# Performance work log

Measured on AMD Instinct MI355X. Metric: run time of the kernel, lower is better.

## Reference

```python
import jax, jax.numpy as jnp
import numpy as np

B, CIN, COUT, H, W, K, S, P = 16, 256, 128, 64, 64, 4, 2, 1
PAD = K - 1 - P  # transposed-conv equivalent padding for the lhs-dilated conv


def setup_inputs() -> dict:
    key = jax.random.key(0)
    ks = jax.random.split(key, 13)
    return {
        "x": jax.random.normal(ks[0], (B, CIN, H, W), jnp.float32),
        "feature": jax.random.uniform(ks[1], (B, 4), jnp.float32),
        "weight": jax.random.normal(ks[2], (CIN, COUT, K, K), jnp.float32) * 0.05,
        "t_bayer": jax.random.normal(ks[3], (1, CIN, COUT, K, K), jnp.float32) * 0.05,
        "t_quad": jax.random.normal(ks[4], (1, CIN, COUT, K, K), jnp.float32) * 0.05,
        "t_nano": jax.random.normal(ks[5], (1, CIN, COUT, K, K), jnp.float32) * 0.05,
        "t_qxq": jax.random.normal(ks[6], (1, CIN, COUT, K, K), jnp.float32) * 0.05,
        "m_bayer": jax.random.uniform(ks[7], (1, CIN, COUT, 1, 1), jnp.float32),
        "m_quad": jax.random.uniform(ks[8], (1, CIN, COUT, 1, 1), jnp.float32),
        "m_nano": jax.random.uniform(ks[9], (1, CIN, COUT, 1, 1), jnp.float32),
        "m_qxq": jax.random.uniform(ks[10], (1, CIN, COUT, 1, 1), jnp.float32),
        "bias": jax.random.normal(ks[11], (COUT,), jnp.float32) * 0.05,
        "prelu_a": jnp.full((1,), 0.25, jnp.float32),
    }


def _synth_weights(feature, weight, t_bayer, t_quad, t_nano, t_qxq,
                   m_bayer, m_quad, m_nano, m_qxq):
    # feature: (B,4) softmax attention -> (B,4,1,1,1)
    sa = feature[:, :, None, None, None]
    dyn = (t_bayer * m_bayer * sa[:, 0:1]
           + t_quad * m_quad * sa[:, 1:2]
           + t_nano * m_nano * sa[:, 2:3]
           + t_qxq * m_qxq * sa[:, 3:4])  # (B, CIN, COUT, K, K)
    return weight[None] + dyn  # broadcast base weight over batch


def _deconv_per_sample(xi, wi):
    # xi: (CIN,H,W); wi: (CIN,COUT,K,K) torch conv_transpose layout.
    # conv_transpose == lhs-dilated conv with spatially-flipped, transposed kernel
    kern = jnp.flip(jnp.swapaxes(wi, 0, 1), axis=(-2, -1))  # (COUT,CIN,K,K)
    out = jax.lax.conv_general_dilated(
        xi[None], kern, window_strides=(1, 1),
        padding=[(PAD, PAD), (PAD, PAD)], lhs_dilation=(S, S),
        dimension_numbers=("NCHW", "OIHW", "NCHW"))
    return out[0]  # (COUT, H*S, W*S)


def reference(x, feature, weight, t_bayer, t_quad, t_nano, t_qxq,
              m_bayer, m_quad, m_nano, m_qxq, bias, prelu_a):
    w = _synth_weights(feature, weight, t_bayer, t_quad, t_nano, t_qxq,
                       m_bayer, m_quad, m_nano, m_qxq)
    out = jax.vmap(_deconv_per_sample)(x, w)  # (B, COUT, 128, 128)
    out = out + bias[None, :, None, None]
    # PReLU with single shared slope (torch default init 0.25)
    return jnp.where(out >= 0, out, prelu_a[0] * out)
```

## Files before the change

kernel.cpp:

```cpp
#include <hip/hip_runtime.h>
#include <hip/hip_bf16.h>
#include <cstddef>
#include <cstdint>

#define B_    16
#define CIN_  256
#define COUT_ 128
#define H_    64
#define W_    64
#define OH_   128
#define OW_   128

typedef __attribute__((ext_vector_type(8))) short bf16x8;
typedef __attribute__((ext_vector_type(4))) float f32x4;

__device__ inline short f2bf(float f) {
    __hip_bfloat16 h = __float2bfloat16(f);
    return *reinterpret_cast<short*>(&h);
}

__device__ inline void async_ld16(const void* g, void* l) {
    typedef const __attribute__((address_space(1))) unsigned int* gp_t;
    typedef __attribute__((address_space(3))) unsigned int* lp_t;
    __builtin_amdgcn_global_load_lds((gp_t)g, (lp_t)l, 16, 0, 0);
}

__global__ __launch_bounds__(256) void synth_aws(
    const float* __restrict__ weight,
    const float* __restrict__ tb, const float* __restrict__ tq,
    const float* __restrict__ tn, const float* __restrict__ tx,
    const float* __restrict__ mb, const float* __restrict__ mq,
    const float* __restrict__ mn, const float* __restrict__ mx,
    const float* __restrict__ feat,
    short* __restrict__ aws)
{
    const int chunk = blockIdx.x;
    const int cog   = blockIdx.y;
    const int b     = blockIdx.z;
    const int tid   = threadIdx.x;
    const int ci0   = chunk * 8;

    __shared__ __align__(16) short lbuf[4][32][40];

    const float f0 = feat[b*4+0], f1 = feat[b*4+1];
    const float f2 = feat[b*4+2], f3 = feat[b*4+3];

    #pragma unroll
    for (int it = 0; it < 4; ++it) {
        int e4   = tid + it*256;
        int ci_l = e4 >> 7;
        int rem  = e4 & 127;
        int co_l = rem >> 2;
        int kh   = rem & 3;
        int co   = cog*32 + co_l;
        int base = (ci0 + ci_l) * COUT_ + co;
        float4 w4 = *(const float4*)(weight + (size_t)base*16 + kh*4);
        float4 b4 = *(const float4*)(tb + (size_t)base*16 + kh*4);
        float4 q4 = *(const float4*)(tq + (size_t)base*16 + kh*4);
        float4 n4 = *(const float4*)(tn + (size_t)base*16 + kh*4);
        float4 x4 = *(const float4*)(tx + (size_t)base*16 + kh*4);
        const float* wp = (const float*)&w4;
        const float* bp = (const float*)&b4;
        const float* qp = (const float*)&q4;
        const float* np = (const float*)&n4;
        const float* xp = (const float*)&x4;
        float sb = mb[base]*f0, sq = mq[base]*f1;
        float sn = mn[base]*f2, sx = mx[base]*f3;
        int r  = (kh+1)&1;
        int dh = (kh<2) ? 1 : 0;
        #pragma unroll
        for (int kw = 0; kw < 4; ++kw) {
            int s  = (kw+1)&1;
            int dw = (kw<2) ? 1 : 0;
            float v = wp[kw] + sb*bp[kw] + sq*qp[kw] + sn*np[kw] + sx*xp[kw];
            lbuf[r*2+s][co_l][(dh*2+dw)*8 + ci_l] = f2bf(v);
        }
    }
    __syncthreads();
    for (int j = tid; j < 640; j += 256) {
        int cls = j / 160; int jj = j - cls*160;
        size_t dst = (((size_t)(b*4 + cls)*32 + chunk)*128 + cog*32) * 40;
        *(int4*)(aws + dst + (size_t)jj*8) = *(const int4*)(&lbuf[cls][0][0] + jj*8);
    }
}

__global__ __launch_bounds__(256) void transform_x(
    const float* __restrict__ x, short* __restrict__ xt)
{
    const int ihp = blockIdx.x;
    const int b   = blockIdx.y;
    const int tid = threadIdx.x;
    const int4 z4 = {0, 0, 0, 0};

    if (ihp == 0 || ihp == 65) {
        for (int j = tid; j < 2112; j += 256) {
            int c = j / 66, iwp = j - c*66;
            *(int4*)(xt + ((((size_t)b*32 + c)*66 + ihp)*66 + iwp)*8) = z4;
        }
        return;
    }
    if (tid < 64) {
        int c = tid >> 1, iwp = (tid & 1) * 65;
        *(int4*)(xt + ((((size_t)b*32 + c)*66 + ihp)*66 + iwp)*8) = z4;
    }
    const int ih = ihp - 1;
    __shared__ float xls[128][64];
    for (int half = 0; half < 2; ++half) {
        __syncthreads();
        #pragma unroll 4
        for (int it = 0; it < 32; ++it) {
            int ci_l = it*4 + (tid >> 6);
            xls[ci_l][tid & 63] =
                x[(((size_t)b*256 + half*128 + ci_l)*64 + ih)*64 + (tid & 63)];
        }
        __syncthreads();
        #pragma unroll
        for (int it2 = 0; it2 < 4; ++it2) {
            int chunk_l = it2*4 + (tid >> 6);
            int chunk   = half*16 + chunk_l;
            int iw      = tid & 63;
            short s8[8];
            #pragma unroll
            for (int j = 0; j < 8; ++j) s8[j] = f2bf(xls[chunk_l*8 + j][iw]);
            *(int4*)(xt + ((((size_t)b*32 + chunk)*66 + ihp)*66 + (iw+1))*8)
                = *(const int4*)s8;
        }
    }
}

__global__ __launch_bounds__(256) void deconv_mfma2(
    const short* __restrict__ aws, const short* __restrict__ xt,
    const float* __restrict__ bias, const float* __restrict__ prelu_a,
    float* __restrict__ out)
{
    const int tid  = threadIdx.x;
    const int lane = tid & 63;
    const int wv   = tid >> 6;
    const int wm   = wv & 1, wn = wv >> 1;
    const int nt   = blockIdx.x;
    const int cls  = blockIdx.y;
    const int b    = blockIdx.z;
    const int a0 = (nt >> 2) * 8, c0 = (nt & 3) * 16;
    const int r = cls >> 1, s = cls & 1;

    __shared__ __align__(16) short als[2][5120];
    __shared__ __align__(16) short xsb[2][1536];

    const short* gb[4]; int gstep[4], loff[4], isB[4], act[4];
    {
        const size_t awb = (((size_t)b*4 + cls)*32) * 5120;
        #pragma unroll
        for (int i = 0; i < 4; ++i) {
            int t = wv + i*4;
            act[i] = (t < 13);
            if (t < 10) {
                gb[i]    = aws + awb + t*512 + lane*8;
                gstep[i] = 5120;  loff[i] = t*512;  isB[i] = 0;
            } else {
                int j = t - 10;
                int p = j*64 + lane; if (p > 152) p = 152;
                int row = p / 17, col = p - row*17;
                gb[i] = xt + (((size_t)b*32*66 + (a0 + r + row))*66
                              + (c0 + s + col)) * 8;
                gstep[i] = 66*66*8;  loff[i] = j*512;  isB[i] = 1;
            }
        }
    }

    f32x4 acc[4][4];
    #pragma unroll
    for (int mi = 0; mi < 4; ++mi)
        #pragma unroll
        for (int ni = 0; ni < 4; ++ni)
            acc[mi][ni] = (f32x4){0.f, 0.f, 0.f, 0.f};

    const int nlo = lane & 15;
    const int q   = lane >> 4;
    const int dh  = q >> 1, dw = q & 1;

    #pragma unroll
    for (int i = 0; i < 4; ++i)
        if (act[i])
            async_ld16(gb[i], isB[i] ? &xsb[0][loff[i]] : &als[0][loff[i]]);

    for (int c = 0; c < 32; ++c) {
        __syncthreads();
        const int sel = c & 1;
        if (c < 31) {
            const int ps = sel ^ 1;
            #pragma unroll
            for (int i = 0; i < 4; ++i)
                if (act[i])
                    async_ld16(gb[i] + (size_t)(c+1)*gstep[i],
                               isB[i] ? &xsb[ps][loff[i]] : &als[ps][loff[i]]);
        }
        bf16x8 af[4], bfr[4];
        #pragma unroll
        for (int mi = 0; mi < 4; ++mi)
            af[mi] = *(const bf16x8*)(&als[sel][(wm*64 + mi*16 + nlo)*40 + q*8]);
        #pragma unroll
        for (int ni = 0; ni < 4; ++ni) {
            int a_local = wn*4 + ni;
            bfr[ni] = *(const bf16x8*)(&xsb[sel][((a_local + dh)*17 + (nlo + dw))*8]);
        }
        #pragma unroll
        for (int mi = 0; mi < 4; ++mi)
            #pragma unroll
            for (int ni = 0; ni < 4; ++ni)
                acc[mi][ni] = __builtin_amdgcn_mfma_f32_16x16x32_bf16(
                    af[mi], bfr[ni], acc[mi][ni], 0, 0, 0);
    }

    const float pa = prelu_a[0];
    #pragma unroll
    for (int mi = 0; mi < 4; ++mi) {
        #pragma unroll
        for (int reg = 0; reg < 4; ++reg) {
            int co = wm*64 + mi*16 + q*4 + reg;
            float bv = bias[co];
            #pragma unroll
            for (int ni = 0; ni < 4; ++ni) {
                int a_local = wn*4 + ni;
                int oh = 2*(a0 + a_local) + r;
                int ow = 2*(c0 + nlo) + s;
                float v = acc[mi][ni][reg] + bv;
                v = (v >= 0.f) ? v : pa*v;
                out[(((size_t)b*COUT_ + co)*OH_ + oh)*OW_ + ow] = v;
            }
        }
    }
}

__global__ __launch_bounds__(256, 2) void deconv_mfma_gather(
    const float* __restrict__ x,
    const short* __restrict__ aws,
    const float* __restrict__ bias,
    const float* __restrict__ prelu_a,
    float* __restrict__ out)
{
    const int tid  = threadIdx.x;
    const int lane = tid & 63;
    const int wv   = tid >> 6;
    const int wm   = wv & 1, wn = wv >> 1;
    const int nt   = blockIdx.x;
    const int cls  = blockIdx.y;
    const int b    = blockIdx.z;
    const int a0 = (nt >> 2) * 8, c0 = (nt & 3) * 16;
    const int r = cls >> 1, s = cls & 1;

    __shared__ __align__(16) short xs[1280];
    __shared__ __align__(16) short als[5120];

    int goff[5], gstep[5], gok[5];
    #pragma unroll
    for (int i = 0; i < 5; ++i) {
        int e    = tid + i*256;
        int ci_l = e & 7;
        int rc   = e >> 3;
        int row  = rc / 17;
        int col  = rc - row*17;
        int ih   = a0 - 1 + r + row;
        int iw   = c0 - 1 + s + col;
        int ok   = (rc < 153) && ((unsigned)ih < (unsigned)H_)
                              && ((unsigned)iw < (unsigned)W_);
        goff[i]  = ok ? (((b*CIN_ + ci_l)*H_ + ih)*W_ + iw) : 0;
        gstep[i] = ok ? (8*H_*W_) : 0;
        gok[i]   = ok;
    }
    const size_t aws_base = (((size_t)b*4 + cls)*32) * 5120;

    f32x4 acc[4][4];
    #pragma unroll
    for (int mi = 0; mi < 4; ++mi)
        #pragma unroll
        for (int ni = 0; ni < 4; ++ni)
            acc[mi][ni] = (f32x4){0.f, 0.f, 0.f, 0.f};

    const int nlo = lane & 15;
    const int q   = lane >> 4;
    const int dh  = q >> 1, dw = q & 1;

    for (int chunk = 0; chunk < 32; ++chunk) {
        __syncthreads();
        #pragma unroll
        for (int i = 0; i < 5; ++i) {
            float v = x[goff[i] + chunk*gstep[i]];
            v = gok[i] ? v : 0.0f;
            xs[tid + i*256] = f2bf(v);
        }
        {
            const short* src = aws + aws_base + (size_t)chunk*5120;
            #pragma unroll
            for (int i = 0; i < 3; ++i) {
                int idx = wv + i*4;
                if (idx < 10)
                    async_ld16(src + idx*512 + lane*8, als + idx*512);
            }
        }
        __syncthreads();
        bf16x8 af[4], bfr[4];
        #pragma unroll
        for (int mi = 0; mi < 4; ++mi)
            af[mi] = *(const bf16x8*)(als + (wm*64 + mi*16 + nlo)*40 + q*8);
        #pragma unroll
        for (int ni = 0; ni < 4; ++ni) {
            int a_local = wn*4 + ni;
            bfr[ni] = *(const bf16x8*)(xs + ((a_local + dh)*17 + (nlo + dw))*8);
        }
        #pragma unroll
        for (int mi = 0; mi < 4; ++mi)
            #pragma unroll
            for (int ni = 0; ni < 4; ++ni)
                acc[mi][ni] = __builtin_amdgcn_mfma_f32_16x16x32_bf16(
                    af[mi], bfr[ni], acc[mi][ni], 0, 0, 0);
    }

    const float pa = prelu_a[0];
    #pragma unroll
    for (int mi = 0; mi < 4; ++mi) {
        #pragma unroll
        for (int reg = 0; reg < 4; ++reg) {
            int co = wm*64 + mi*16 + q*4 + reg;
            float bv = bias[co];
            #pragma unroll
            for (int ni = 0; ni < 4; ++ni) {
                int a_local = wn*4 + ni;
                int oh = 2*(a0 + a_local) + r;
                int ow = 2*(c0 + nlo) + s;
                float v = acc[mi][ni][reg] + bv;
                v = (v >= 0.f) ? v : pa*v;
                out[(((size_t)b*COUT_ + co)*OH_ + oh)*OW_ + ow] = v;
            }
        }
    }
}

__global__ __launch_bounds__(256) void deconv_fallback(
    const float* __restrict__ x,
    const float* __restrict__ weight,
    const float* __restrict__ tb, const float* __restrict__ tq,
    const float* __restrict__ tn, const float* __restrict__ tx,
    const float* __restrict__ mb, const float* __restrict__ mq,
    const float* __restrict__ mn, const float* __restrict__ mx,
    const float* __restrict__ feat,
    const float* __restrict__ bias, const float* __restrict__ prelu_a,
    float* __restrict__ out)
{
    const int tid    = threadIdx.x;
    const int tile   = blockIdx.x;
    const int coT    = blockIdx.y;
    const int b      = blockIdx.z;
    const int tile_h = tile >> 3, tile_w = tile & 7;
    const int a0 = tile_h * 8;
    const int c0 = tile_w * 8;
    const int co0 = coT * 64;

    const int tco = tid & 15;
    const int tpx = tid >> 4;
    const int rr  = tpx >> 2, rc = tpx & 3;

    __shared__ float xsf[4][100];
    __shared__ float wsh[4][16][64];

    float acc[4][4][4];
    #pragma unroll
    for (int i = 0; i < 4; ++i)
        #pragma unroll
        for (int j = 0; j < 4; ++j)
            #pragma unroll
            for (int c = 0; c < 4; ++c) acc[i][j][c] = 0.f;

    float f0 = feat[b*4 + 0], f1 = feat[b*4 + 1];
    float f2 = feat[b*4 + 2], f3 = feat[b*4 + 3];

    for (int chunk = 0; chunk < CIN_ / 4; ++chunk) {
        const int ci0 = chunk * 4;
        __syncthreads();
        for (int e = tid; e < 400; e += 256) {
            int ci_l = e / 100; int rem = e - ci_l * 100;
            int rI = rem / 10;  int cI = rem - rI * 10;
            int ih = a0 - 1 + rI, iw = c0 - 1 + cI;
            float v = 0.f;
            if ((unsigned)ih < (unsigned)H_ && (unsigned)iw < (unsigned)W_)
                v = x[(((size_t)b * CIN_ + ci0 + ci_l) * H_ + ih) * W_ + iw];
            xsf[ci_l][rem] = v;
        }
        #pragma unroll
        for (int k = 0; k < 4; ++k) {
            int g = tid + k * 256;
            int ci_l = g >> 8; int rrem = g & 255;
            int co_l = rrem >> 2; int tg = (rrem & 3) * 4;
            int cico = (ci0 + ci_l) * COUT_ + co0 + co_l;
            int e = cico * 16 + tg;
            float4 w  = *(const float4*)(weight + e);
            float4 vb = *(const float4*)(tb + e);
            float4 vq = *(const float4*)(tq + e);
            float4 vn = *(const float4*)(tn + e);
            float4 vx = *(const float4*)(tx + e);
            float sb = mb[cico] * f0, sq = mq[cico] * f1;
            float sn = mn[cico] * f2, sx = mx[cico] * f3;
            float4 wvv;
            wvv.x = w.x + sb*vb.x + sq*vq.x + sn*vn.x + sx*vx.x;
            wvv.y = w.y + sb*vb.y + sq*vq.y + sn*vn.y + sx*vx.y;
            wvv.z = w.z + sb*vb.z + sq*vq.z + sn*vn.z + sx*vx.z;
            wvv.w = w.w + sb*vb.w + sq*vq.w + sn*vn.w + sx*vx.w;
            wsh[ci_l][tg + 0][co_l] = wvv.x;
            wsh[ci_l][tg + 1][co_l] = wvv.y;
            wsh[ci_l][tg + 2][co_l] = wvv.z;
            wsh[ci_l][tg + 3][co_l] = wvv.w;
        }
        __syncthreads();
        #pragma unroll
        for (int ci_l = 0; ci_l < 4; ++ci_l) {
            float xpv[4][4];
            #pragma unroll
            for (int i = 0; i < 4; ++i)
                #pragma unroll
                for (int j = 0; j < 4; ++j)
                    xpv[i][j] = xsf[ci_l][(rr*2 + i) * 10 + rc*2 + j];
            #pragma unroll
            for (int kh = 0; kh < 4; ++kh) {
                const int rpar = (kh & 1) ? 0 : 1;
                const int offh = (kh == 0) ? 2 : (kh == 3) ? 0 : 1;
                #pragma unroll
                for (int kw = 0; kw < 4; ++kw) {
                    const int spar = (kw & 1) ? 0 : 1;
                    const int offw = (kw == 0) ? 2 : (kw == 3) ? 0 : 1;
                    float4 wvv = *(const float4*)&wsh[ci_l][kh*4 + kw][tco*4];
                    float wr[4] = {wvv.x, wvv.y, wvv.z, wvv.w};
                    #pragma unroll
                    for (int da = 0; da < 2; ++da)
                        #pragma unroll
                        for (int dc = 0; dc < 2; ++dc) {
                            const float xvv = xpv[da + offh][dc + offw];
                            #pragma unroll
                            for (int cc = 0; cc < 4; ++cc)
                                acc[2*da + rpar][2*dc + spar][cc] =
                                    fmaf(wr[cc], xvv, acc[2*da + rpar][2*dc + spar][cc]);
                        }
                }
            }
        }
    }
    const float pa  = prelu_a[0];
    const int oh0 = tile_h * 16 + rr * 4;
    const int ow0 = tile_w * 16 + rc * 4;
    #pragma unroll
    for (int cc = 0; cc < 4; ++cc) {
        const int co = co0 + tco * 4 + cc;
        const float bv = bias[co];
        #pragma unroll
        for (int dr = 0; dr < 4; ++dr)
            #pragma unroll
            for (int dw2 = 0; dw2 < 4; ++dw2) {
                float v = acc[dr][dw2][cc] + bv;
                v = (v >= 0.f) ? v : pa * v;
                out[(((size_t)b * COUT_ + co) * OH_ + (oh0 + dr)) * OW_ + (ow0 + dw2)] = v;
            }
    }
}

extern "C" void kernel_launch(void* const* d_in, const int* in_sizes, int n_in,
                              void* d_out, int out_size, void* d_ws, size_t ws_size,
                              hipStream_t stream) {
    (void)in_sizes; (void)n_in; (void)out_size;
    const float* x      = (const float*)d_in[0];
    const float* feat   = (const float*)d_in[1];
    const float* weight = (const float*)d_in[2];
    const float* tb     = (const float*)d_in[3];
    const float* tq     = (const float*)d_in[4];
    const float* tn     = (const float*)d_in[5];
    const float* tx     = (const float*)d_in[6];
    const float* mb     = (const float*)d_in[7];
    const float* mq     = (const float*)d_in[8];
    const float* mn     = (const float*)d_in[9];
    const float* mx     = (const float*)d_in[10];
    const float* bias   = (const float*)d_in[11];
    const float* prelu  = (const float*)d_in[12];
    float* out = (float*)d_out;

    const size_t aws_sz = (size_t)B_ * 4 * 32 * 128 * 40 * sizeof(short);
    const size_t xt_sz  = (size_t)B_ * 32 * 66 * 66 * 8 * sizeof(short);

    if (ws_size >= aws_sz + xt_sz) {
        short* aws = (short*)d_ws;
        short* xt  = (short*)((char*)d_ws + aws_sz);
        synth_aws<<<dim3(32, 4, 16), 256, 0, stream>>>(
            weight, tb, tq, tn, tx, mb, mq, mn, mx, feat, aws);
        transform_x<<<dim3(66, 16), 256, 0, stream>>>(x, xt);
        deconv_mfma2<<<dim3(32, 4, 16), 256, 0, stream>>>(
            aws, xt, bias, prelu, out);
    } else if (ws_size >= aws_sz) {
        short* aws = (short*)d_ws;
        synth_aws<<<dim3(32, 4, 16), 256, 0, stream>>>(
            weight, tb, tq, tn, tx, mb, mq, mn, mx, feat, aws);
        deconv_mfma_gather<<<dim3(32, 4, 16), 256, 0, stream>>>(
            x, aws, bias, prelu, out);
    } else {
        deconv_fallback<<<dim3(64, 2, 16), 256, 0, stream>>>(
            x, weight, tb, tq, tn, tx, mb, mq, mn, mx, feat, bias, prelu, out);
    }
}
```

Before: 297.8 us.

## Fuse prep kernels, pad weight LDS stride, vectorize x loads, swizzle deconv grid

Merges the weight-synthesis and x-transform kernels into one launch that picks its role by block index, removing a launch and letting both prep jobs overlap. The weight tile row stride grows from 40 to 44 shorts to cut LDS bank conflicts on the MFMA A-fragment reads, at the cost of a larger workspace and one extra async load per chunk. The x transform now uses float4 global loads into a padded shared tile. The deconv grid is flattened and remapped so consecutive blocks spread across batch and class, which may change L2 locality.

```diff
diff --git a/kernel.cpp b/kernel.cpp
--- a/kernel.cpp
+++ b/kernel.cpp
@@ -11,6 +11,10 @@
 #define OH_   128
 #define OW_   128
 
+#define AST   44
+#define ACHUNK (128*AST)
+#define ABYTES (ACHUNK*2)
+
 typedef __attribute__((ext_vector_type(8))) short bf16x8;
 typedef __attribute__((ext_vector_type(4))) float f32x4;
 
@@ -25,23 +29,18 @@
     __builtin_amdgcn_global_load_lds((gp_t)g, (lp_t)l, 16, 0, 0);
 }
 
-__global__ __launch_bounds__(256) void synth_aws(
+__device__ inline void synth_body(
+    int chunk, int cog, int b, int tid,
     const float* __restrict__ weight,
     const float* __restrict__ tb, const float* __restrict__ tq,
     const float* __restrict__ tn, const float* __restrict__ tx,
     const float* __restrict__ mb, const float* __restrict__ mq,
     const float* __restrict__ mn, const float* __restrict__ mx,
     const float* __restrict__ feat,
-    short* __restrict__ aws)
-{
-    const int chunk = blockIdx.x;
-    const int cog   = blockIdx.y;
-    const int b     = blockIdx.z;
-    const int tid   = threadIdx.x;
-    const int ci0   = chunk * 8;
-
-    __shared__ __align__(16) short lbuf[4][32][40];
-
+    short* __restrict__ aws,
+    short* lbuf )
+{
+    const int ci0 = chunk * 8;
     const float f0 = feat[b*4+0], f1 = feat[b*4+1];
     const float f2 = feat[b*4+2], f3 = feat[b*4+3];
 
@@ -73,23 +72,23 @@
             int s  = (kw+1)&1;
             int dw = (kw<2) ? 1 : 0;
             float v = wp[kw] + sb*bp[kw] + sq*qp[kw] + sn*np[kw] + sx*xp[kw];
-            lbuf[r*2+s][co_l][(dh*2+dw)*8 + ci_l] = f2bf(v);
+            lbuf[((r*2+s)*32 + co_l)*AST + (dh*2+dw)*8 + ci_l] = f2bf(v);
         }
     }
     __syncthreads();
-    for (int j = tid; j < 640; j += 256) {
-        int cls = j / 160; int jj = j - cls*160;
-        size_t dst = (((size_t)(b*4 + cls)*32 + chunk)*128 + cog*32) * 40;
-        *(int4*)(aws + dst + (size_t)jj*8) = *(const int4*)(&lbuf[cls][0][0] + jj*8);
-    }
-}
-
-__global__ __launch_bounds__(256) void transform_x(
-    const float* __restrict__ x, short* __restrict__ xt)
-{
-    const int ihp = blockIdx.x;
-    const int b   = blockIdx.y;
-    const int tid = threadIdx.x;
+    for (int j = tid; j < 4*176; j += 256) {
+        int cls = j / 176; int jj = j - cls*176;
+        size_t dst = (((size_t)(b*4 + cls)*32 + chunk)*128 + cog*32) * AST;
+        *(int4*)(aws + dst + (size_t)jj*8) =
+            *(const int4*)(lbuf + cls*32*AST + jj*8);
+    }
+}
+
+__device__ inline void transform_body(
+    int ihp, int b, int tid,
+    const float* __restrict__ x, short* __restrict__ xt,
+    float* xls )
+{
     const int4 z4 = {0, 0, 0, 0};
 
     if (ihp == 0 || ihp == 65) {
@@ -104,14 +103,15 @@
         *(int4*)(xt + ((((size_t)b*32 + c)*66 + ihp)*66 + iwp)*8) = z4;
     }
     const int ih = ihp - 1;
-    __shared__ float xls[128][64];
     for (int half = 0; half < 2; ++half) {
         __syncthreads();
-        #pragma unroll 4
-        for (int it = 0; it < 32; ++it) {
-            int ci_l = it*4 + (tid >> 6);
-            xls[ci_l][tid & 63] =
-                x[(((size_t)b*256 + half*128 + ci_l)*64 + ih)*64 + (tid & 63)];
+        #pragma unroll
+        for (int it = 0; it < 8; ++it) {
+            int ci_l = it*16 + (tid >> 4);
+            int iw4  = (tid & 15) * 4;
+            float4 v = *(const float4*)(
+                x + (((size_t)b*256 + half*128 + ci_l)*64 + ih)*64 + iw4);
+            *(float4*)(xls + ci_l*68 + iw4) = v;
         }
         __syncthreads();
         #pragma unroll
@@ -121,16 +121,163 @@
             int iw      = tid & 63;
             short s8[8];
             #pragma unroll
-            for (int j = 0; j < 8; ++j) s8[j] = f2bf(xls[chunk_l*8 + j][iw]);
+            for (int j = 0; j < 8; ++j)
+                s8[j] = f2bf(xls[(chunk_l*8 + j)*68 + iw]);
             *(int4*)(xt + ((((size_t)b*32 + chunk)*66 + ihp)*66 + (iw+1))*8)
                 = *(const int4*)s8;
         }
     }
+}
+
+__global__ __launch_bounds__(256) void prep_fused(
+    const float* __restrict__ x,
+    const float* __restrict__ weight,
+    const float* __restrict__ tb, const float* __restrict__ tq,
+    const float* __restrict__ tn, const float* __restrict__ tx,
+    const float* __restrict__ mb, const float* __restrict__ mq,
+    const float* __restrict__ mn, const float* __restrict__ mx,
+    const float* __restrict__ feat,
+    short* __restrict__ aws, short* __restrict__ xt)
+{
+    __shared__ __align__(16) char smem[34816];
+    const int bid = blockIdx.x;
+    const int tid = threadIdx.x;
+    if (bid < 1056) {
+        int ihp = bid % 66, b = bid / 66;
+        transform_body(ihp, b, tid, x, xt, (float*)smem);
+    } else {
+        int sb = bid - 1056;
+        int chunk = sb & 31, cog = (sb >> 5) & 3, b = sb >> 7;
+        synth_body(chunk, cog, b, tid, weight, tb, tq, tn, tx,
+                   mb, mq, mn, mx, feat, aws, (short*)smem);
+    }
+}
+
+__global__ __launch_bounds__(256) void synth_aws(
+    const float* __restrict__ weight,
+    const float* __restrict__ tb, const float* __restrict__ tq,
+    const float* __restrict__ tn, const float* __restrict__ tx,
+    const float* __restrict__ mb, const float* __restrict__ mq,
+    const float* __restrict__ mn, const float* __restrict__ mx,
+    const float* __restrict__ feat,
+    short* __restrict__ aws)
+{
+    __shared__ __align__(16) short lbuf[4][32][AST];
+    const int chunk = blockIdx.x, cog = blockIdx.y, b = blockIdx.z;
+    synth_body(chunk, cog, b, threadIdx.x, weight, tb, tq, tn, tx,
+               mb, mq, mn, mx, feat, aws, &lbuf[0][0][0]);
 }
 
 __global__ __launch_bounds__(256) void deconv_mfma2(
     const short* __restrict__ aws, const short* __restrict__ xt,
     const float* __restrict__ bias, const float* __restrict__ prelu_a,
+    float* __restrict__ out)
+{
+    const int tid  = threadIdx.x;
+    const int lane = tid & 63;
+    const int wv   = tid >> 6;
+    const int wm   = wv & 1, wn = wv >> 1;
+    const int o    = blockIdx.x;
+    const int n    = (o & 7) * 256 + (o >> 3);
+    const int nt   = n & 31;
+    const int cls  = (n >> 5) & 3;
+    const int b    = n >> 7;
+    const int a0 = (nt >> 2) * 8, c0 = (nt & 3) * 16;
+    const int r = cls >> 1, s = cls & 1;
+
+    __shared__ __align__(16) short als[2][ACHUNK];
+    __shared__ __align__(16) short xsb[2][1536];
+
+    const short* gb[4]; int gstep[4], loff[4], isB[4], act[4];
+    {
+        const size_t awb = (((size_t)b*4 + cls)*32) * ACHUNK;
+        #pragma unroll
+        for (int i = 0; i < 4; ++i) {
+            int t = wv + i*4;
+            act[i] = (t < 14);
+            if (t < 11) {
+                gb[i]    = aws + awb + t*512 + lane*8;
+                gstep[i] = ACHUNK;  loff[i] = t*512;  isB[i] = 0;
+            } else {
+                int j = t - 11;
+                int p = j*64 + lane; if (p > 152) p = 152;
+                int row = p / 17, col = p - row*17;
+                gb[i] = xt + (((size_t)b*32*66 + (a0 + r + row))*66
+                              + (c0 + s + col)) * 8;
+                gstep[i] = 66*66*8;  loff[i] = j*512;  isB[i] = 1;
+            }
+        }
+    }
+
+    f32x4 acc[4][4];
+    #pragma unroll
+    for (int mi = 0; mi < 4; ++mi)
+        #pragma unroll
+        for (int ni = 0; ni < 4; ++ni)
+            acc[mi][ni] = (f32x4){0.f, 0.f, 0.f, 0.f};
+
+    const int nlo = lane & 15;
+    const int q   = lane >> 4;
+    const int dh  = q >> 1, dw = q & 1;
+
+    #pragma unroll
+    for (int i = 0; i < 4; ++i)
+        if (act[i])
+            async_ld16(gb[i], isB[i] ? &xsb[0][loff[i]] : &als[0][loff[i]]);
+
+    for (int c = 0; c < 32; ++c) {
+        __syncthreads();
+        const int sel = c & 1;
+        if (c < 31) {
+            const int ps = sel ^ 1;
+            #pragma unroll
+            for (int i = 0; i < 4; ++i)
+                if (act[i])
+                    async_ld16(gb[i] + (size_t)(c+1)*gstep[i],
+                               isB[i] ? &xsb[ps][loff[i]] : &als[ps][loff[i]]);
+        }
+        bf16x8 af[4], bfr[4];
+        #pragma unroll
+        for (int mi = 0; mi < 4; ++mi)
+            af[mi] = *(const bf16x8*)(&als[sel][(wm*64 + mi*16 + nlo)*AST + q*8]);
+        #pragma unroll
+        for (int ni = 0; ni < 4; ++ni) {
+            int a_local = wn*4 + ni;
+            bfr[ni] = *(const bf16x8*)(&xsb[sel][((a_local + dh)*17 + (nlo + dw))*8]);
+        }
+        #pragma unroll
+        for (int mi = 0; mi < 4; ++mi)
+            #pragma unroll
+            for (int ni = 0; ni < 4; ++ni)
+                acc[mi][ni] = __builtin_amdgcn_mfma_f32_16x16x32_bf16(
+                    af[mi], bfr[ni], acc[mi][ni], 0, 0, 0);
+    }
+
+    const float pa = prelu_a[0];
+    #pragma unroll
+    for (int mi = 0; mi < 4; ++mi) {
+        #pragma unroll
+        for (int reg = 0; reg < 4; ++reg) {
+            int co = wm*64 + mi*16 + q*4 + reg;
+            float bv = bias[co];
+            #pragma unroll
+            for (int ni = 0; ni < 4; ++ni) {
+                int a_local = wn*4 + ni;
+                int oh = 2*(a0 + a_local) + r;
+                int ow = 2*(c0 + nlo) + s;
+                float v = acc[mi][ni][reg] + bv;
+                v = (v >= 0.f) ? v : pa*v;
+                out[(((size_t)b*COUT_ + co)*OH_ + oh)*OW_ + ow] = v;
+            }
+        }
+    }
+}
+
+__global__ __launch_bounds__(256, 2) void deconv_mfma_gather(
+    const float* __restrict__ x,
+    const short* __restrict__ aws,
+    const float* __restrict__ bias,
+    const float* __restrict__ prelu_a,
     float* __restrict__ out)
 {
     const int tid  = threadIdx.x;
@@ -143,113 +290,8 @@
     const int a0 = (nt >> 2) * 8, c0 = (nt & 3) * 16;
     const int r = cls >> 1, s = cls & 1;
 
-    __shared__ __align__(16) short als[2][5120];
-    __shared__ __align__(16) short xsb[2][1536];
-
-    const short* gb[4]; int gstep[4], loff[4], isB[4], act[4];
-    {
-        const size_t awb = (((size_t)b*4 + cls)*32) * 5120;
-        #pragma unroll
-        for (int i = 0; i < 4; ++i) {
-            int t = wv + i*4;
-            act[i] = (t < 13);
-            if (t < 10) {
-                gb[i]    = aws + awb + t*512 + lane*8;
-                gstep[i] = 5120;  loff[i] = t*512;  isB[i] = 0;
-            } else {
-                int j = t - 10;
-                int p = j*64 + lane; if (p > 152) p = 152;
-                int row = p / 17, col = p - row*17;
-                gb[i] = xt + (((size_t)b*32*66 + (a0 + r + row))*66
-                              + (c0 + s + col)) * 8;
-                gstep[i] = 66*66*8;  loff[i] = j*512;  isB[i] = 1;
-            }
-        }
-    }
-
-    f32x4 acc[4][4];
-    #pragma unroll
-    for (int mi = 0; mi < 4; ++mi)
-        #pragma unroll
-        for (int ni = 0; ni < 4; ++ni)
-            acc[mi][ni] = (f32x4){0.f, 0.f, 0.f, 0.f};
-
-    const int nlo = lane & 15;
-    const int q   = lane >> 4;
-    const int dh  = q >> 1, dw = q & 1;
-
-    #pragma unroll
-    for (int i = 0; i < 4; ++i)
-        if (act[i])
-            async_ld16(gb[i], isB[i] ? &xsb[0][loff[i]] : &als[0][loff[i]]);
-
-    for (int c = 0; c < 32; ++c) {
-        __syncthreads();
-        const int sel = c & 1;
-        if (c < 31) {
-            const int ps = sel ^ 1;
-            #pragma unroll
-            for (int i = 0; i < 4; ++i)
-                if (act[i])
-                    async_ld16(gb[i] + (size_t)(c+1)*gstep[i],
-                               isB[i] ? &xsb[ps][loff[i]] : &als[ps][loff[i]]);
-        }
-        bf16x8 af[4], bfr[4];
-        #pragma unroll
-        for (int mi = 0; mi < 4; ++mi)
-            af[mi] = *(const bf16x8*)(&als[sel][(wm*64 + mi*16 + nlo)*40 + q*8]);
-        #pragma unroll
-        for (int ni = 0; ni < 4; ++ni) {
-            int a_local = wn*4 + ni;
-            bfr[ni] = *(const bf16x8*)(&xsb[sel][((a_local + dh)*17 + (nlo + dw))*8]);
-        }
-        #pragma unroll
-        for (int mi = 0; mi < 4; ++mi)
-            #pragma unroll
-            for (int ni = 0; ni < 4; ++ni)
-                acc[mi][ni] = __builtin_amdgcn_mfma_f32_16x16x32_bf16(
-                    af[mi], bfr[ni], acc[mi][ni], 0, 0, 0);
-    }
-
-    const float pa = prelu_a[0];
-    #pragma unroll
-    for (int mi = 0; mi < 4; ++mi) {
-        #pragma unroll
-        for (int reg = 0; reg < 4; ++reg) {
-            int co = wm*64 + mi*16 + q*4 + reg;
-            float bv = bias[co];
-            #pragma unroll
-            for (int ni = 0; ni < 4; ++ni) {
-                int a_local = wn*4 + ni;
-                int oh = 2*(a0 + a_local) + r;
-                int ow = 2*(c0 + nlo) + s;
-                float v = acc[mi][ni][reg] + bv;
-                v = (v >= 0.f) ? v : pa*v;
-                out[(((size_t)b*COUT_ + co)*OH_ + oh)*OW_ + ow] = v;
-            }
-        }
-    }
-}
-
-__global__ __launch_bounds__(256, 2) void deconv_mfma_gather(
-    const float* __restrict__ x,
-    const short* __restrict__ aws,
-    const float* __restrict__ bias,
-    const float* __restrict__ prelu_a,
-    float* __restrict__ out)
-{
-    const int tid  = threadIdx.x;
-    const int lane = tid & 63;
-    const int wv   = tid >> 6;
-    const int wm   = wv & 1, wn = wv >> 1;
-    const int nt   = blockIdx.x;
-    const int cls  = blockIdx.y;
-    const int b    = blockIdx.z;
-    const int a0 = (nt >> 2) * 8, c0 = (nt & 3) * 16;
-    const int r = cls >> 1, s = cls & 1;
-
     __shared__ __align__(16) short xs[1280];
-    __shared__ __align__(16) short als[5120];
+    __shared__ __align__(16) short als[ACHUNK];
 
     int goff[5], gstep[5], gok[5];
     #pragma unroll
@@ -267,7 +309,7 @@
         gstep[i] = ok ? (8*H_*W_) : 0;
         gok[i]   = ok;
     }
-    const size_t aws_base = (((size_t)b*4 + cls)*32) * 5120;
+    const size_t aws_base = (((size_t)b*4 + cls)*32) * ACHUNK;
 
     f32x4 acc[4][4];
     #pragma unroll
@@ -289,11 +331,11 @@
             xs[tid + i*256] = f2bf(v);
         }
         {
-            const short* src = aws + aws_base + (size_t)chunk*5120;
+            const short* src = aws + aws_base + (size_t)chunk*ACHUNK;
             #pragma unroll
             for (int i = 0; i < 3; ++i) {
                 int idx = wv + i*4;
-                if (idx < 10)
+                if (idx < 11)
                     async_ld16(src + idx*512 + lane*8, als + idx*512);
             }
         }
@@ -301,7 +343,7 @@
         bf16x8 af[4], bfr[4];
         #pragma unroll
         for (int mi = 0; mi < 4; ++mi)
-            af[mi] = *(const bf16x8*)(als + (wm*64 + mi*16 + nlo)*40 + q*8);
+            af[mi] = *(const bf16x8*)(als + (wm*64 + mi*16 + nlo)*AST + q*8);
         #pragma unroll
         for (int ni = 0; ni < 4; ++ni) {
             int a_local = wn*4 + ni;
@@ -479,16 +521,15 @@
     const float* prelu  = (const float*)d_in[12];
     float* out = (float*)d_out;
 
-    const size_t aws_sz = (size_t)B_ * 4 * 32 * 128 * 40 * sizeof(short);
+    const size_t aws_sz = (size_t)B_ * 4 * 32 * 128 * AST * sizeof(short);
     const size_t xt_sz  = (size_t)B_ * 32 * 66 * 66 * 8 * sizeof(short);
 
     if (ws_size >= aws_sz + xt_sz) {
         short* aws = (short*)d_ws;
         short* xt  = (short*)((char*)d_ws + aws_sz);
-        synth_aws<<<dim3(32, 4, 16), 256, 0, stream>>>(
-            weight, tb, tq, tn, tx, mb, mq, mn, mx, feat, aws);
-        transform_x<<<dim3(66, 16), 256, 0, stream>>>(x, xt);
-        deconv_mfma2<<<dim3(32, 4, 16), 256, 0, stream>>>(
+        prep_fused<<<dim3(1056 + 2048), 256, 0, stream>>>(
+            x, weight, tb, tq, tn, tx, mb, mq, mn, mx, feat, aws, xt);
+        deconv_mfma2<<<dim3(2048), 256, 0, stream>>>(
             aws, xt, bias, prelu, out);
     } else if (ws_size >= aws_sz) {
         short* aws = (short*)d_ws;
```

Result: slower. 321.0 us (+7.8%).
